# Optimization experiments

Hardware: AMD Instinct MI355X
Metric: run time of the kernel (lower is better)

Reference implementation:

```python
import jax, jax.numpy as jnp
import numpy as np
from jax import lax

B, T, S, D = 16, 16, 196, 768
H = 256          # hidden_dim
NH = 4           # attention heads
TH = 32          # temporal hidden = max(16, H//8)
UP = 4           # UPSAMPLE_FACTOR


def _ln(x, w, b):
    m = jnp.mean(x, -1, keepdims=True)
    v = jnp.mean((x - m) ** 2, -1, keepdims=True)
    return (x - m) / jnp.sqrt(v + 1e-5) * w + b


def _gelu(x):
    return jax.nn.gelu(x, approximate=False)  # torch nn.GELU default (erf)


def _upmat(g, f):
    # torch F.interpolate bilinear, align_corners=False, as a [g*f, g] matrix
    g_up = g * f
    src = np.maximum((np.arange(g_up) + 0.5) / f - 0.5, 0.0)
    i0 = np.minimum(np.floor(src).astype(np.int64), g - 1)
    i1 = np.minimum(i0 + 1, g - 1)
    w1 = (src - i0).astype(np.float32)
    w0 = 1.0 - w1
    W = np.zeros((g_up, g), dtype=np.float32)
    np.add.at(W, (np.arange(g_up), i0), w0)
    np.add.at(W, (np.arange(g_up), i1), w1)
    return jnp.asarray(W)


def setup_inputs() -> dict:
    key = jax.random.key(0)
    ks = jax.random.split(key, 12)
    r = lambda i, shape: jax.random.normal(ks[i], shape, jnp.float32) * 0.02
    return dict(
        tokens=jax.random.normal(ks[0], (B, T * S, D), jnp.float32),
        num_frames=T,
        fixed_box_wh=jax.random.uniform(ks[1], (2,), jnp.float32, 0.1, 0.5),
        ln_w=jnp.ones((D,), jnp.float32), ln_b=jnp.zeros((D,), jnp.float32),
        query=r(2, (1, 1, D)),
        in_proj_w=r(3, (3 * D, D)), in_proj_b=jnp.zeros((3 * D,), jnp.float32),
        out_w=r(4, (D, D)), out_b=jnp.zeros((D,), jnp.float32),
        an_w=jnp.ones((D,), jnp.float32), an_b=jnp.zeros((D,), jnp.float32),
        obj_w=r(5, (1, D)), obj_b=jnp.zeros((1,), jnp.float32),
        temperature=jnp.asarray(8.0, jnp.float32),
        r1_w=r(6, (H, 2 * D)), r1_b=jnp.zeros((H,), jnp.float32),
        r2_w=r(7, (H // 2, H)), r2_b=jnp.zeros((H // 2,), jnp.float32),
        r3_w=r(8, (2, H // 2)), r3_b=jnp.zeros((2,), jnp.float32),
        tc1_w=r(9, (TH, 2, 5)), tc1_b=jnp.zeros((TH,), jnp.float32),
        tc2_w=r(10, (2, TH, 5)), tc2_b=jnp.zeros((2,), jnp.float32),
    )


def reference(tokens, num_frames, fixed_box_wh, ln_w, ln_b, query,
              in_proj_w, in_proj_b, out_w, out_b, an_w, an_b, obj_w, obj_b,
              temperature, r1_w, r1_b, r2_w, r2_b, r3_w, r3_b,
              tc1_w, tc1_b, tc2_w, tc2_b):
    Bb, N, Dd = tokens.shape
    Tt = int(num_frames)
    Ss = N // Tt
    g = int(round(Ss ** 0.5))
    g_up = g * UP
    BT = Bb * Tt
    dt = tokens.dtype

    normed = _ln(tokens, ln_w, ln_b)
    flat = normed.reshape(BT, Ss, Dd)  # per-frame tokens

    # --- attention pooling with learned query (dropout off, eval) ---
    Wq, Wk, Wv = jnp.split(in_proj_w, 3, 0)
    bq, bk, bv = jnp.split(in_proj_b, 3, 0)
    dh = Dd // NH
    qh = (query.reshape(1, Dd) @ Wq.T + bq).reshape(NH, dh)  # same query for all frames
    kh = (flat @ Wk.T + bk).reshape(BT, Ss, NH, dh)
    vh = (flat @ Wv.T + bv).reshape(BT, Ss, NH, dh)
    scores = jnp.einsum('hd,bshd->bhs', qh, kh) / jnp.sqrt(jnp.asarray(dh, dt))
    attnp = jax.nn.softmax(scores, -1)
    ctx = jnp.einsum('bhs,bshd->bhd', attnp, vh).reshape(BT, Dd)
    pooled = _ln(ctx @ out_w.T + out_b, an_w, an_b)

    obj = (flat @ obj_w.T + obj_b)[..., 0]  # [BT,S]
    Wu = _upmat(g, UP)
    up = jnp.einsum('ug,bgh,vh->buv', Wu, obj.reshape(BT, g, g), Wu)
    up = up.reshape(BT, g_up * g_up)
    temp = jnp.maximum(temperature, 1.0)
    probs = jax.nn.softmax(up * temp, -1)
    coords = (jnp.arange(g_up, dtype=dt) + 0.5) / g_up
    yy, xx = jnp.meshgrid(coords, coords, indexing='ij')
    cx0 = probs @ xx.reshape(-1)
    cy0 = probs @ yy.reshape(-1)

    # --- 3x3 local token gather around coarse center ---
    cxg = jnp.clip(cx0 * g, 0, g - 1).astype(jnp.int32)
    cyg = jnp.clip(cy0 * g, 0, g - 1).astype(jnp.int32)
    off = jnp.array([-1, 0, 1], jnp.int32)
    gy = jnp.clip(cyg[:, None, None] + off[None, :, None], 0, g - 1)
    gx = jnp.clip(cxg[:, None, None] + off[None, None, :], 0, g - 1)
    idx = (gy * g + gx).reshape(BT, 9)
    local = jnp.take_along_axis(flat, idx[:, :, None], axis=1).mean(1)

    # --- refine MLP ---
    h1 = _gelu(jnp.concatenate([pooled, local], -1) @ r1_w.T + r1_b)
    h2 = _gelu(h1 @ r2_w.T + r2_b)
    delta = h2 @ r3_w.T + r3_b
    cx = jnp.clip(cx0 + 0.3 * jnp.tanh(delta[:, 0]), 0.0, 1.0)
    cy = jnp.clip(cy0 + 0.3 * jnp.tanh(delta[:, 1]), 0.0, 1.0)

    # --- temporal residual refiner over center trajectories ---
    seq = jnp.stack([cx, cy], 1).reshape(Bb, Tt, 2).transpose(0, 2, 1)  # [B,2,T]
    dn = ('NCH', 'OIH', 'NCH')
    t1 = _gelu(lax.conv_general_dilated(seq, tc1_w, (1,), [(2, 2)],
                                        dimension_numbers=dn) + tc1_b[None, :, None])
    td = lax.conv_general_dilated(t1, tc2_w, (1,), [(2, 2)],
                                  dimension_numbers=dn) + tc2_b[None, :, None]
    td = td.transpose(0, 2, 1).reshape(BT, 2)
    cx = jnp.clip(cx + 0.12 * jnp.tanh(td[:, 0]), 0.0, 1.0)
    cy = jnp.clip(cy + 0.12 * jnp.tanh(td[:, 1]), 0.0, 1.0)

    # --- fixed-size boxes ---
    min_size = 1.0 / g
    wh = jnp.clip(jnp.broadcast_to(fixed_box_wh.reshape(1, 2), (Bb, 2)), min_size, 1.0)
    wh = jnp.broadcast_to(wh[:, None, :], (Bb, Tt, 2)).reshape(BT, 2)
    w, h = wh[:, 0], wh[:, 1]
    x1 = jnp.clip(cx - 0.5 * w, 0.0, 1.0)
    y1 = jnp.clip(cy - 0.5 * h, 0.0, 1.0)
    x2 = jnp.clip(cx + 0.5 * w, 0.0, 1.0)
    y2 = jnp.clip(cy + 0.5 * h, 0.0, 1.0)
    x2 = jnp.clip(jnp.maximum(x2, x1 + min_size), 0.0, 1.0)
    y2 = jnp.clip(jnp.maximum(y2, y1 + min_size), 0.0, 1.0)
    return jnp.stack([x1, y1, x2, y2], 1).reshape(Bb, Tt, 4)
```

## Files before the change

### kernel.cpp

```cpp
#include <hip/hip_runtime.h>
#include <hip/hip_bf16.h>
#include <math.h>

#define SS 196
#define DD 768

__device__ __forceinline__ float b2f(ushort u){
  union { unsigned int i; float f; } v; v.i = ((unsigned int)u) << 16; return v.f;
}
__device__ __forceinline__ bool bfmode(const void* lnw){
  return ((const ushort*)lnw)[0] != 0;
}
__device__ __forceinline__ float ldx(const void* p, size_t i, bool bf){
  return bf ? b2f(((const ushort*)p)[i]) : ((const float*)p)[i];
}
__device__ __forceinline__ float gelu_f(float x){
  return 0.5f * x * (1.0f + erff(x * 0.70710678118654752f));
}
__device__ __forceinline__ float wredsum(float v){
  #pragma unroll
  for(int o=32;o;o>>=1) v += __shfl_xor(v,o,64);
  return v;
}
__device__ __forceinline__ float wredmax(float v){
  #pragma unroll
  for(int o=32;o;o>>=1) v = fmaxf(v, __shfl_xor(v,o,64));
  return v;
}

__global__ __launch_bounds__(256) void k_wkpart(const void* __restrict__ wproj,
                                                const void* __restrict__ query,
                                                const void* __restrict__ bproj,
                                                const void* __restrict__ flagp,
                                                float* __restrict__ wkp){
  bool bf = bfmode(flagp);
  int bx = blockIdx.x, c = blockIdx.y;
  int tid = threadIdx.x;
  int wv = tid>>6, lane = tid&63;
  int h = bx/3;
  __shared__ float sqh[12];
  #pragma unroll
  for(int j = wv*3; j < wv*3+3; j++){
    int rr = h*192 + c*12 + j;
    float acc = 0.f;
    #pragma unroll
    for(int i=0;i<12;i++){ int d = lane + 64*i; acc += ldx(query,d,bf) * ldx(wproj,(size_t)rr*DD+d,bf); }
    acc = wredsum(acc);
    if(lane==0) sqh[j] = acc + ldx(bproj, rr, bf);
  }
  __syncthreads();
  int idx = bx*256 + tid;
  int d = idx - h*DD;
  size_t base = ((size_t)(DD + h*192 + c*12))*DD + d;
  float acc = 0.f;
  #pragma unroll
  for(int j=0;j<12;j++) acc += sqh[j] * ldx(wproj, base + (size_t)j*DD, bf);
  wkp[(size_t)c*3072 + idx] = acc;
}

__global__ __launch_bounds__(256) void k_wkcomb(const float* __restrict__ wkp,
                                                const void* __restrict__ lnw,
                                                const void* __restrict__ lnb,
                                                const void* __restrict__ objw,
                                                float* __restrict__ wkraw,
                                                float* __restrict__ wf,
                                                float* __restrict__ s12p){
  bool bf = bfmode(lnw);
  int bx = blockIdx.x;
  int idx = bx*256 + threadIdx.x;
  int h = idx / DD, d = idx - h*DD;
  float s = 0.f;
  #pragma unroll
  for(int c=0;c<16;c++) s += wkp[(size_t)c*3072 + idx];
  wkraw[idx] = s;
  float w = ldx(lnw,d,bf);
  float wfv = w * s;
  wf[idx] = wfv;
  float lb = ldx(lnb,d,bf);
  float p0 = wfv;
  float p5 = lb * s;
  float p4 = 0.f, p9 = 0.f;
  if(bx < 3){
    float ow = ldx(objw,d,bf);
    float wfo = w * ow;
    wf[4*DD + d] = wfo;
    p4 = wfo;
    p9 = lb * ow;
  }
  p0 = wredsum(p0); p5 = wredsum(p5); p4 = wredsum(p4); p9 = wredsum(p9);
  __shared__ float red[4][4];
  int wv = threadIdx.x>>6, lane = threadIdx.x&63;
  if(lane==0){ red[0][wv]=p0; red[1][wv]=p5; red[2][wv]=p4; red[3][wv]=p9; }
  __syncthreads();
  if(threadIdx.x==0){
    float q0=red[0][0]+red[0][1]+red[0][2]+red[0][3];
    float q5=red[1][0]+red[1][1]+red[1][2]+red[1][3];
    float q4=red[2][0]+red[2][1]+red[2][2]+red[2][3];
    float q9=red[3][0]+red[3][1]+red[3][2]+red[3][3];
    #pragma unroll
    for(int r=0;r<10;r++) s12p[bx*10+r]=0.f;
    s12p[bx*10 + h] = q0;
    s12p[bx*10 + 5 + h] = q5;
    if(bx<3){ s12p[bx*10 + 4] = q4; s12p[bx*10 + 9] = q9; }
  }
}

__global__ __launch_bounds__(256) void k_pass1(const void* __restrict__ tok,
                                               const float* __restrict__ wf,
                                               const float* __restrict__ s12p,
                                               const void* __restrict__ objb,
                                               const void* __restrict__ flagp,
                                               float* __restrict__ scores,
                                               float* __restrict__ objv,
                                               float* __restrict__ meanv,
                                               float* __restrict__ rstdv){
  __shared__ __align__(16) float swf[5*DD];
  __shared__ float ss12[10];
  for(int i=threadIdx.x;i<5*DD;i+=256) swf[i]=wf[i];
  if(threadIdx.x<10){
    float a=0.f;
    #pragma unroll
    for(int b=0;b<12;b++) a += s12p[b*10+threadIdx.x];
    ss12[threadIdx.x]=a;
  }
  __syncthreads();
  bool bf = bfmode(flagp);
  int tid = threadIdx.x;
  int tl = tid & 15;
  int tkn = blockIdx.x*16 + (tid>>4);
  int f = tkn / SS, s = tkn - f*SS;
  float a0=0,a1=0,a2=0,a3=0,a4=0,sm=0,sq=0;
  if(bf){
    const ushort* x = (const ushort*)tok + (size_t)tkn * DD;
    #pragma unroll
    for(int i=0;i<12;i++){
      int d = 4*tl + 64*i;
      ushort4 u = *(const ushort4*)(x + d);
      float x0=b2f(u.x), x1=b2f(u.y), x2=b2f(u.z), x3=b2f(u.w);
      sm += (x0+x1)+(x2+x3); sq += (x0*x0+x1*x1)+(x2*x2+x3*x3);
      float4 w;
      w = *(const float4*)&swf[0*DD+d]; a0 += x0*w.x + x1*w.y + x2*w.z + x3*w.w;
      w = *(const float4*)&swf[1*DD+d]; a1 += x0*w.x + x1*w.y + x2*w.z + x3*w.w;
      w = *(const float4*)&swf[2*DD+d]; a2 += x0*w.x + x1*w.y + x2*w.z + x3*w.w;
      w = *(const float4*)&swf[3*DD+d]; a3 += x0*w.x + x1*w.y + x2*w.z + x3*w.w;
      w = *(const float4*)&swf[4*DD+d]; a4 += x0*w.x + x1*w.y + x2*w.z + x3*w.w;
    }
  } else {
    const float* x = (const float*)tok + (size_t)tkn * DD;
    #pragma unroll
    for(int i=0;i<12;i++){
      int d = 4*tl + 64*i;
      float4 u = *(const float4*)(x + d);
      sm += (u.x+u.y)+(u.z+u.w);
      sq += (u.x*u.x+u.y*u.y)+(u.z*u.z+u.w*u.w);
      float4 w;
      w = *(const float4*)&swf[0*DD+d]; a0 += u.x*w.x+u.y*w.y+u.z*w.z+u.w*w.w;
      w = *(const float4*)&swf[1*DD+d]; a1 += u.x*w.x+u.y*w.y+u.z*w.z+u.w*w.w;
      w = *(const float4*)&swf[2*DD+d]; a2 += u.x*w.x+u.y*w.y+u.z*w.z+u.w*w.w;
      w = *(const float4*)&swf[3*DD+d]; a3 += u.x*w.x+u.y*w.y+u.z*w.z+u.w*w.w;
      w = *(const float4*)&swf[4*DD+d]; a4 += u.x*w.x+u.y*w.y+u.z*w.z+u.w*w.w;
    }
  }
  #pragma unroll
  for(int o=8;o;o>>=1){
    sm += __shfl_xor(sm,o,64); sq += __shfl_xor(sq,o,64);
    a0 += __shfl_xor(a0,o,64); a1 += __shfl_xor(a1,o,64);
    a2 += __shfl_xor(a2,o,64); a3 += __shfl_xor(a3,o,64);
    a4 += __shfl_xor(a4,o,64);
  }
  if(tl==0){
    const float invD = 1.0f/768.0f;
    float m = sm*invD;
    float var = sq*invD - m*m;
    float rstd = rsqrtf(var + 1e-5f);
    meanv[tkn]=m; rstdv[tkn]=rstd;
    const float sc = 0.07216878364870322f;
    scores[(f*4+0)*SS+s] = (rstd*(a0 - m*ss12[0]) + ss12[5]) * sc;
    scores[(f*4+1)*SS+s] = (rstd*(a1 - m*ss12[1]) + ss12[6]) * sc;
    scores[(f*4+2)*SS+s] = (rstd*(a2 - m*ss12[2]) + ss12[7]) * sc;
    scores[(f*4+3)*SS+s] = (rstd*(a3 - m*ss12[3]) + ss12[8]) * sc;
    objv[tkn] = rstd*(a4 - m*ss12[4]) + ss12[9] + ldx(objb,0,bf);
  }
}

__global__ __launch_bounds__(512) void k_softobj(const void* __restrict__ tok,
                                                 float* __restrict__ aw,
                                                 const float* __restrict__ objv,
                                                 const float* __restrict__ meanv,
                                                 const float* __restrict__ rstdv,
                                                 const void* __restrict__ temp,
                                                 const void* __restrict__ lnw,
                                                 const void* __restrict__ lnb,
                                                 float* __restrict__ pl,
                                                 float* __restrict__ cterm,
                                                 float* __restrict__ cxy){
  bool bf = bfmode(lnw);
  int f = blockIdx.x, tid = threadIdx.x;
  int wv = tid >> 6, lane = tid & 63;
  __shared__ float sobj[196];
  __shared__ float up[3136];
  __shared__ int   i0a[56], i1a[56];
  __shared__ float w0a[56], w1a[56];
  __shared__ float redm[4], reds[8], redx[8], redy[8];
  __shared__ int   sidx[9];
  __shared__ float rj[9], rmj[9];
  if(tid<196) sobj[tid] = objv[(size_t)f*SS + tid];
  if(tid<56){
    float src = fmaxf((tid+0.5f)*0.25f - 0.5f, 0.0f);
    int i0 = min((int)floorf(src), 13);
    i0a[tid]=i0; i1a[tid]=min(i0+1,13);
    float w1 = src - (float)i0;
    w1a[tid]=w1; w0a[tid]=1.0f-w1;
  }
  __syncthreads();
  if(wv < 4){
    int h = wv;
    float* sc = aw + (size_t)(f*4+h)*SS;
    const float* rs = rstdv + f*SS;
    const float* mv = meanv + f*SS;
    float v[4]; float mx = -1e30f;
    #pragma unroll
    for(int j=0;j<4;j++){ int s=lane+64*j; v[j] = (s<SS)? sc[s] : -1e30f; mx=fmaxf(mx,v[j]); }
    mx = wredmax(mx);
    float e[4], sum=0.f;
    #pragma unroll
    for(int j=0;j<4;j++){ int s=lane+64*j; e[j] = (s<SS)? expf(v[j]-mx) : 0.f; sum += e[j]; }
    sum = wredsum(sum);
    float inv = 1.0f/sum;
    float cp = 0.f;
    #pragma unroll
    for(int j=0;j<4;j++){
      int s=lane+64*j;
      if(s<SS){ float r=rs[s]; float a=e[j]*inv*r; sc[s]=a; cp += a*mv[s]; }
    }
    cp = wredsum(cp);
    if(lane==0) cterm[f*4+h] = cp;
  } else {
    int w4 = wv-4;
    float lmax = -1e30f;
    for(int i = w4*64 + lane; i<3136; i+=256){
      int u=i/56, v=i-u*56;
      float val = w0a[u]*(w0a[v]*sobj[i0a[u]*14+i0a[v]] + w1a[v]*sobj[i0a[u]*14+i1a[v]])
                + w1a[u]*(w0a[v]*sobj[i1a[u]*14+i0a[v]] + w1a[v]*sobj[i1a[u]*14+i1a[v]]);
      up[i]=val; lmax=fmaxf(lmax,val);
    }
    lmax = wredmax(lmax);
    if(lane==0) redm[w4]=lmax;
  }
  __syncthreads();
  float mx = fmaxf(fmaxf(redm[0],redm[1]), fmaxf(redm[2],redm[3]));
  float t = fmaxf(ldx(temp,0,bf), 1.0f);
  float se=0, sx=0, sy=0;
  for(int i=tid;i<3136;i+=512){
    int u=i/56, v=i-u*56;
    float e = expf((up[i]-mx)*t);
    se += e;
    sx += e * ((v+0.5f)*(1.0f/56.0f));
    sy += e * ((u+0.5f)*(1.0f/56.0f));
  }
  se=wredsum(se); sx=wredsum(sx); sy=wredsum(sy);
  if(lane==0){ reds[wv]=se; redx[wv]=sx; redy[wv]=sy; }
  __syncthreads();
  se=0; sx=0; sy=0;
  #pragma unroll
  for(int i=0;i<8;i++){ se+=reds[i]; sx+=redx[i]; sy+=redy[i]; }
  float cx0 = sx/se, cy0 = sy/se;
  if(tid==0){ cxy[f*2]=cx0; cxy[f*2+1]=cy0; }
  float vx = fminf(fmaxf(cx0*14.0f,0.0f),13.0f); int cxg=(int)vx;
  float vy = fminf(fmaxf(cy0*14.0f,0.0f),13.0f); int cyg=(int)vy;
  if(tid<9){
    int dy = tid/3 - 1, dx = tid%3 - 1;
    int gy = min(max(cyg+dy,0),13), gx = min(max(cxg+dx,0),13);
    int s = gy*14+gx;
    sidx[tid]=s;
    float r = rstdv[(size_t)f*SS+s];
    rj[tid]=r; rmj[tid]=r*meanv[(size_t)f*SS+s];
  }
  __syncthreads();
  float offc = 0.f;
  #pragma unroll
  for(int j=0;j<9;j++) offc += rmj[j];
  for(int d=tid; d<DD; d+=512){
    float acc = 0.f;
    #pragma unroll
    for(int j=0;j<9;j++) acc += rj[j]*ldx(tok, (size_t)f*SS*DD + (size_t)sidx[j]*DD + d, bf);
    pl[(size_t)f*1536 + DD + d] = ldx(lnw,d,bf)*((acc-offc)*(1.0f/9.0f)) + ldx(lnb,d,bf);
  }
}

__global__ __launch_bounds__(256) void k_xbar_part(const void* __restrict__ tok,
                                                   const float* __restrict__ aw,
                                                   const void* __restrict__ flagp,
                                                   float* __restrict__ xpart){
  bool bf = bfmode(flagp);
  int f = blockIdx.x, c = blockIdx.y;
  __shared__ float a4[49*4];
  for(int i=threadIdx.x;i<49*4;i+=256){
    int s=i>>2, h=i&3;
    a4[i]=aw[(size_t)(f*4+h)*SS + c*49 + s];
  }
  __syncthreads();
  int tid = threadIdx.x;
  if(tid < 192){
    int d = tid*4;
    float4 A0={0,0,0,0},A1={0,0,0,0},A2={0,0,0,0},A3={0,0,0,0};
    if(bf){
      const ushort* tf = (const ushort*)tok + (size_t)(f*SS + c*49)*DD + d;
      #pragma unroll 7
      for(int s=0;s<49;s++){
        ushort4 u = *(const ushort4*)(tf + (size_t)s*DD);
        float x0=b2f(u.x), x1=b2f(u.y), x2=b2f(u.z), x3=b2f(u.w);
        float w0=a4[s*4+0], w1=a4[s*4+1], w2=a4[s*4+2], w3=a4[s*4+3];
        A0.x+=w0*x0; A0.y+=w0*x1; A0.z+=w0*x2; A0.w+=w0*x3;
        A1.x+=w1*x0; A1.y+=w1*x1; A1.z+=w1*x2; A1.w+=w1*x3;
        A2.x+=w2*x0; A2.y+=w2*x1; A2.z+=w2*x2; A2.w+=w2*x3;
        A3.x+=w3*x0; A3.y+=w3*x1; A3.z+=w3*x2; A3.w+=w3*x3;
      }
    } else {
      const float* tf = (const float*)tok + (size_t)(f*SS + c*49)*DD + d;
      #pragma unroll 7
      for(int s=0;s<49;s++){
        float4 u = *(const float4*)(tf + (size_t)s*DD);
        float w0=a4[s*4+0], w1=a4[s*4+1], w2=a4[s*4+2], w3=a4[s*4+3];
        A0.x+=w0*u.x; A0.y+=w0*u.y; A0.z+=w0*u.z; A0.w+=w0*u.w;
        A1.x+=w1*u.x; A1.y+=w1*u.y; A1.z+=w1*u.z; A1.w+=w1*u.w;
        A2.x+=w2*u.x; A2.y+=w2*u.y; A2.z+=w2*u.z; A2.w+=w2*u.w;
        A3.x+=w3*u.x; A3.y+=w3*u.y; A3.z+=w3*u.z; A3.w+=w3*u.w;
      }
    }
    size_t base = (((size_t)c*256 + f)*4)*DD + d;
    *(float4*)&xpart[base + 0*DD] = A0;
    *(float4*)&xpart[base + 1*DD] = A1;
    *(float4*)&xpart[base + 2*DD] = A2;
    *(float4*)&xpart[base + 3*DD] = A3;
  }
}

__global__ __launch_bounds__(256) void k_xbar_comb(const float* __restrict__ xpart,
                                                   const float* __restrict__ cterm,
                                                   const void* __restrict__ lnw,
                                                   const void* __restrict__ lnb,
                                                   float* __restrict__ xbar){
  bool bf = bfmode(lnw);
  int f = blockIdx.x;
  float c0=cterm[f*4+0], c1=cterm[f*4+1], c2=cterm[f*4+2], c3=cterm[f*4+3];
  #pragma unroll
  for(int j=0;j<3;j++){
    int d = threadIdx.x + 256*j;
    float w=ldx(lnw,d,bf), b=ldx(lnb,d,bf);
    float s0=0,s1=0,s2=0,s3=0;
    #pragma unroll
    for(int c=0;c<4;c++){
      size_t base = (((size_t)c*256 + f)*4)*DD + d;
      s0 += xpart[base + 0*DD];
      s1 += xpart[base + 1*DD];
      s2 += xpart[base + 2*DD];
      s3 += xpart[base + 3*DD];
    }
    xbar[((size_t)(f*4+0))*DD+d] = w*(s0-c0)+b;
    xbar[((size_t)(f*4+1))*DD+d] = w*(s1-c1)+b;
    xbar[((size_t)(f*4+2))*DD+d] = w*(s2-c2)+b;
    xbar[((size_t)(f*4+3))*DD+d] = w*(s3-c3)+b;
  }
}

template<int N, int K, int ACT, int CTX, int ROWOFF>
__global__ __launch_bounds__(256) void k_tgemm(const float* __restrict__ A,
                                               const void* __restrict__ W,
                                               const void* __restrict__ bias,
                                               const void* __restrict__ flagp,
                                               float* __restrict__ C){
  bool bf = bfmode(flagp);
  __shared__ float As[32][32];
  __shared__ float Bs[32][64];
  int tid = threadIdx.x;
  int n0 = blockIdx.x*64, m0 = blockIdx.y*32;
  int h  = n0 / 192;
  int am = tid>>3, ak = (tid&7)*4;
  int bn = tid>>2, bk = (tid&3)*8;
  const float* ap = A + (CTX ? ((size_t)((m0+am)*4+h))*768 : (size_t)(m0+am)*K) + ak;
  const ushort* wpb = (const ushort*)W + (size_t)(ROWOFF+n0+bn)*K + bk;
  const float*  wpf = (const float*)W  + (size_t)(ROWOFF+n0+bn)*K + bk;
  int tx = tid&15, ty = tid>>4;
  float acc[2][4] = {};
  float4 av; float b8[8];
  av = *(const float4*)ap;
  if(bf){
    ushort4 w0 = *(const ushort4*)(wpb);
    ushort4 w1 = *(const ushort4*)(wpb+4);
    b8[0]=b2f(w0.x); b8[1]=b2f(w0.y); b8[2]=b2f(w0.z); b8[3]=b2f(w0.w);
    b8[4]=b2f(w1.x); b8[5]=b2f(w1.y); b8[6]=b2f(w1.z); b8[7]=b2f(w1.w);
  } else {
    float4 w0 = *(const float4*)(wpf);
    float4 w1 = *(const float4*)(wpf+4);
    b8[0]=w0.x; b8[1]=w0.y; b8[2]=w0.z; b8[3]=w0.w;
    b8[4]=w1.x; b8[5]=w1.y; b8[6]=w1.z; b8[7]=w1.w;
  }
  for(int k0=0; k0<K; k0+=32){
    As[ak+0][am]=av.x; As[ak+1][am]=av.y; As[ak+2][am]=av.z; As[ak+3][am]=av.w;
    #pragma unroll
    for(int j=0;j<8;j++) Bs[bk+j][bn]=b8[j];
    __syncthreads();
    float4 av2; float b82[8];
    if(k0+32 < K){
      av2 = *(const float4*)(ap + k0 + 32);
      if(bf){
        ushort4 w0 = *(const ushort4*)(wpb + k0 + 32);
        ushort4 w1 = *(const ushort4*)(wpb + k0 + 36);
        b82[0]=b2f(w0.x); b82[1]=b2f(w0.y); b82[2]=b2f(w0.z); b82[3]=b2f(w0.w);
        b82[4]=b2f(w1.x); b82[5]=b2f(w1.y); b82[6]=b2f(w1.z); b82[7]=b2f(w1.w);
      } else {
        float4 w0 = *(const float4*)(wpf + k0 + 32);
        float4 w1 = *(const float4*)(wpf + k0 + 36);
        b82[0]=w0.x; b82[1]=w0.y; b82[2]=w0.z; b82[3]=w0.w;
        b82[4]=w1.x; b82[5]=w1.y; b82[6]=w1.z; b82[7]=w1.w;
      }
    }
    #pragma unroll
    for(int k=0;k<32;k++){
      float2 a = *(const float2*)&As[k][ty*2];
      float4 b = *(const float4*)&Bs[k][tx*4];
      acc[0][0]+=a.x*b.x; acc[0][1]+=a.x*b.y; acc[0][2]+=a.x*b.z; acc[0][3]+=a.x*b.w;
      acc[1][0]+=a.y*b.x; acc[1][1]+=a.y*b.y; acc[1][2]+=a.y*b.z; acc[1][3]+=a.y*b.w;
    }
    __syncthreads();
    av = av2;
    #pragma unroll
    for(int j=0;j<8;j++) b8[j]=b82[j];
  }
  int n = n0 + tx*4;
  float bv0=ldx(bias,ROWOFF+n,bf),   bv1=ldx(bias,ROWOFF+n+1,bf),
        bv2=ldx(bias,ROWOFF+n+2,bf), bv3=ldx(bias,ROWOFF+n+3,bf);
  #pragma unroll
  for(int i=0;i<2;i++){
    int m = m0 + ty*2 + i;
    float4 o;
    o.x=acc[i][0]+bv0; o.y=acc[i][1]+bv1; o.z=acc[i][2]+bv2; o.w=acc[i][3]+bv3;
    if(ACT){ o.x=gelu_f(o.x); o.y=gelu_f(o.y); o.z=gelu_f(o.z); o.w=gelu_f(o.w); }
    *(float4*)&C[(size_t)m*N + n] = o;
  }
}

__global__ __launch_bounds__(256) void k_lnan(const float* __restrict__ X,
                                              const void* __restrict__ anw,
                                              const void* __restrict__ anb,
                                              const void* __restrict__ flagp,
                                              float* __restrict__ pl){
  bool bf = bfmode(flagp);
  int wv = threadIdx.x >> 6, lane = threadIdx.x & 63;
  int f = blockIdx.x*4 + wv;
  const float* x = X + (size_t)f*DD;
  float v[12]; float sm=0, sq=0;
  #pragma unroll
  for(int i=0;i<12;i++){ v[i]=x[lane+64*i]; sm+=v[i]; sq+=v[i]*v[i]; }
  sm=wredsum(sm); sq=wredsum(sq);
  float m = sm*(1.0f/768.0f);
  float rstd = rsqrtf(sq*(1.0f/768.0f) - m*m + 1e-5f);
  #pragma unroll
  for(int i=0;i<12;i++){
    int d = lane+64*i;
    pl[(size_t)f*1536 + d] = (v[i]-m)*rstd*ldx(anw,d,bf) + ldx(anb,d,bf);
  }
}

__global__ __launch_bounds__(256) void k_final(const float* __restrict__ h2,
                                               const void* __restrict__ r3w,
                                               const void* __restrict__ r3b,
                                               const float* __restrict__ cxy,
                                               const void* __restrict__ tc1w,
                                               const void* __restrict__ tc1b,
                                               const void* __restrict__ tc2w,
                                               const void* __restrict__ tc2b,
                                               const void* __restrict__ fbw,
                                               const void* __restrict__ flagp,
                                               void* __restrict__ out){
  bool bf = bfmode(flagp);
  __shared__ float sxs[256], sys[256];
  __shared__ float t1[16*32*16];
  __shared__ float td[16*2*16];
  int f = threadIdx.x;
  float a0=0.f, a1=0.f;
  const float* hh = h2 + (size_t)f*128;
  for(int k=0;k<128;k++){ float x=hh[k]; a0 += x*ldx(r3w,k,bf); a1 += x*ldx(r3w,128+k,bf); }
  a0 += ldx(r3b,0,bf); a1 += ldx(r3b,1,bf);
  float cx1 = fminf(fmaxf(cxy[f*2]   + 0.3f*tanhf(a0), 0.f), 1.f);
  float cy1 = fminf(fmaxf(cxy[f*2+1] + 0.3f*tanhf(a1), 0.f), 1.f);
  sxs[f]=cx1; sys[f]=cy1;
  __syncthreads();
  for(int idx=f; idx<8192; idx+=256){
    int b = idx>>9, o = (idx>>4)&31, t = idx&15;
    float acc = ldx(tc1b,o,bf);
    #pragma unroll
    for(int k=0;k<5;k++){
      int tt = t + k - 2;
      if(tt>=0 && tt<16)
        acc += sxs[b*16+tt]*ldx(tc1w,o*10 + k,bf) + sys[b*16+tt]*ldx(tc1w,o*10 + 5 + k,bf);
    }
    t1[idx] = gelu_f(acc);
  }
  __syncthreads();
  for(int idx=f; idx<512; idx+=256){
    int b = idx>>5, c = (idx>>4)&1, t = idx&15;
    float acc = ldx(tc2b,c,bf);
    for(int o=0;o<32;o++){
      #pragma unroll
      for(int k=0;k<5;k++){
        int tt = t + k - 2;
        if(tt>=0 && tt<16) acc += t1[(b*32+o)*16+tt]*ldx(tc2w,(c*32+o)*5+k,bf);
      }
    }
    td[(b*2+c)*16+t] = acc;
  }
  __syncthreads();
  {
    int b = f>>4;
    float tdx = td[(b*2+0)*16+(f&15)], tdy = td[(b*2+1)*16+(f&15)];
    float cx2 = fminf(fmaxf(sxs[f] + 0.12f*tanhf(tdx), 0.f), 1.f);
    float cy2 = fminf(fmaxf(sys[f] + 0.12f*tanhf(tdy), 0.f), 1.f);
    const float ms = 1.0f/14.0f;
    float w  = fminf(fmaxf(ldx(fbw,0,bf), ms), 1.f);
    float ht = fminf(fmaxf(ldx(fbw,1,bf), ms), 1.f);
    float x1 = fminf(fmaxf(cx2 - 0.5f*w , 0.f), 1.f);
    float y1 = fminf(fmaxf(cy2 - 0.5f*ht, 0.f), 1.f);
    float x2 = fminf(fmaxf(cx2 + 0.5f*w , 0.f), 1.f);
    float y2 = fminf(fmaxf(cy2 + 0.5f*ht, 0.f), 1.f);
    x2 = fminf(fmaxf(fmaxf(x2, x1+ms), 0.f), 1.f);
    y2 = fminf(fmaxf(fmaxf(y2, y1+ms), 0.f), 1.f);
    if(bf){
      __hip_bfloat16* ob = (__hip_bfloat16*)out;
      ob[f*4+0]=__float2bfloat16(x1);
      ob[f*4+1]=__float2bfloat16(y1);
      ob[f*4+2]=__float2bfloat16(x2);
      ob[f*4+3]=__float2bfloat16(y2);
    } else {
      float* of = (float*)out;
      of[f*4+0]=x1; of[f*4+1]=y1; of[f*4+2]=x2; of[f*4+3]=y2;
    }
  }
}

extern "C" void kernel_launch(void* const* d_in, const int* in_sizes, int n_in,
                              void* d_out, int out_size, void* d_ws, size_t ws_size,
                              hipStream_t stream){
  (void)in_sizes; (void)n_in; (void)out_size; (void)ws_size;
  const void* tok   = d_in[0];
  const void* fbw   = d_in[2];
  const void* lnw   = d_in[3];
  const void* lnb   = d_in[4];
  const void* query = d_in[5];
  const void* wproj = d_in[6];
  const void* bproj = d_in[7];
  const void* outw  = d_in[8];
  const void* outb  = d_in[9];
  const void* anw   = d_in[10];
  const void* anb   = d_in[11];
  const void* objw  = d_in[12];
  const void* objb  = d_in[13];
  const void* temp  = d_in[14];
  const void* r1w   = d_in[15];
  const void* r1b   = d_in[16];
  const void* r2w   = d_in[17];
  const void* r2b   = d_in[18];
  const void* r3w   = d_in[19];
  const void* r3b   = d_in[20];
  const void* tc1w  = d_in[21];
  const void* tc1b  = d_in[22];
  const void* tc2w  = d_in[23];
  const void* tc2b  = d_in[24];

  float* ws    = (float*)d_ws;
  float* wkraw = ws;
  float* wf    = wkraw + 3072;
  float* s12p  = wf + 3840;
  float* wkp   = s12p + 128;
  float* scores= wkp + 49152;
  float* objv  = scores + 200704;
  float* meanv = objv + 50176;
  float* rstdv = meanv + 50176;
  float* cterm = rstdv + 50176;
  float* xbar  = cterm + 1024;
  float* ctx   = xbar + 786432;
  float* ppre  = ctx + 196608;
  float* pl    = ppre + 196608;
  float* h1    = pl + 393216;
  float* h2    = h1 + 65536;
  float* cxy   = h2 + 32768;
  float* xpart = cxy + 512;

  hipLaunchKernelGGL(k_wkpart, dim3(12,16),  dim3(256), 0, stream, wproj, query, bproj, lnw, wkp);
  hipLaunchKernelGGL(k_wkcomb, dim3(12),     dim3(256), 0, stream, wkp, lnw, lnb, objw, wkraw, wf, s12p);
  hipLaunchKernelGGL(k_pass1,  dim3(3136),   dim3(256), 0, stream, tok, wf, s12p, objb, lnw, scores, objv, meanv, rstdv);
  hipLaunchKernelGGL(k_softobj,dim3(256),    dim3(512), 0, stream, tok, scores, objv, meanv, rstdv, temp, lnw, lnb, pl, cterm, cxy);
  hipLaunchKernelGGL(k_xbar_part, dim3(256,4), dim3(256), 0, stream, tok, scores, lnw, xpart);
  hipLaunchKernelGGL(k_xbar_comb, dim3(256),   dim3(256), 0, stream, xpart, cterm, lnw, lnb, xbar);
  hipLaunchKernelGGL((k_tgemm<768,768,0,1,1536>), dim3(12,8), dim3(256), 0, stream, xbar, wproj, bproj, lnw, ctx);
  hipLaunchKernelGGL((k_tgemm<768,768,0,0,0>),    dim3(12,8), dim3(256), 0, stream, ctx, outw, outb, lnw, ppre);
  hipLaunchKernelGGL(k_lnan,   dim3(64),     dim3(256), 0, stream, ppre, anw, anb, lnw, pl);
  hipLaunchKernelGGL((k_tgemm<256,1536,1,0,0>), dim3(4,8), dim3(256), 0, stream, pl, r1w, r1b, lnw, h1);
  hipLaunchKernelGGL((k_tgemm<128,256,1,0,0>),  dim3(2,8), dim3(256), 0, stream, h1, r2w, r2b, lnw, h2);
  hipLaunchKernelGGL(k_final,  dim3(1),      dim3(256), 0, stream, h2, r3w, r3b, cxy, tc1w, tc1b, tc2w, tc2b, fbw, lnw, (void*)d_out);
}
```

Before: 505.1 us.

## Fuse softmax/objectness into xbar partial kernel and fold xbar combine into ctx GEMM

Merges the softmax/objectness kernel and the xbar partial-sum kernel into one launch with a (256,5) grid. Every block recomputes the per-head softmax weights into shared memory. Block c==0 handles the objectness upsample, centroid and local pooling, while the other blocks do the weighted token reductions. The xbar combine kernel is removed: the ctx GEMM now sums the four partials and applies the LN affine and cterm correction while loading its A tile. This drops two launches and the xbar round trip, at the cost of redundant softmax work and a heavier A-load in the GEMM.

Result: slower. 521.3 us (+3.2%).

```diff
diff --git a/kernel.cpp b/kernel.cpp
--- a/kernel.cpp
+++ b/kernel.cpp
@@ -183,39 +183,42 @@
   }
 }
 
-__global__ __launch_bounds__(512) void k_softobj(const void* __restrict__ tok,
-                                                 float* __restrict__ aw,
-                                                 const float* __restrict__ objv,
-                                                 const float* __restrict__ meanv,
-                                                 const float* __restrict__ rstdv,
-                                                 const void* __restrict__ temp,
-                                                 const void* __restrict__ lnw,
-                                                 const void* __restrict__ lnb,
-                                                 float* __restrict__ pl,
-                                                 float* __restrict__ cterm,
-                                                 float* __restrict__ cxy){
+__global__ __launch_bounds__(256) void k_attn(const void* __restrict__ tok,
+                                              const float* __restrict__ scores,
+                                              const float* __restrict__ objv,
+                                              const float* __restrict__ meanv,
+                                              const float* __restrict__ rstdv,
+                                              const void* __restrict__ temp,
+                                              const void* __restrict__ lnw,
+                                              const void* __restrict__ lnb,
+                                              float* __restrict__ xpart,
+                                              float* __restrict__ pl,
+                                              float* __restrict__ cterm,
+                                              float* __restrict__ cxy){
   bool bf = bfmode(lnw);
-  int f = blockIdx.x, tid = threadIdx.x;
-  int wv = tid >> 6, lane = tid & 63;
+  int f = blockIdx.x, c = blockIdx.y;
+  int tid = threadIdx.x, wv = tid>>6, lane = tid&63;
+  __shared__ float a4[SS*4];
   __shared__ float sobj[196];
   __shared__ float up[3136];
   __shared__ int   i0a[56], i1a[56];
   __shared__ float w0a[56], w1a[56];
-  __shared__ float redm[4], reds[8], redx[8], redy[8];
+  __shared__ float redm[4], reds[4], redx[4], redy[4];
   __shared__ int   sidx[9];
   __shared__ float rj[9], rmj[9];
-  if(tid<196) sobj[tid] = objv[(size_t)f*SS + tid];
-  if(tid<56){
-    float src = fmaxf((tid+0.5f)*0.25f - 0.5f, 0.0f);
-    int i0 = min((int)floorf(src), 13);
-    i0a[tid]=i0; i1a[tid]=min(i0+1,13);
-    float w1 = src - (float)i0;
-    w1a[tid]=w1; w0a[tid]=1.0f-w1;
-  }
-  __syncthreads();
-  if(wv < 4){
+  if(c==0){
+    if(tid<196) sobj[tid] = objv[(size_t)f*SS + tid];
+    if(tid<56){
+      float src = fmaxf((tid+0.5f)*0.25f - 0.5f, 0.0f);
+      int i0 = min((int)floorf(src), 13);
+      i0a[tid]=i0; i1a[tid]=min(i0+1,13);
+      float w1 = src - (float)i0;
+      w1a[tid]=w1; w0a[tid]=1.0f-w1;
+    }
+  }
+  {
     int h = wv;
-    float* sc = aw + (size_t)(f*4+h)*SS;
+    const float* sc = scores + (size_t)(f*4+h)*SS;
     const float* rs = rstdv + f*SS;
     const float* mv = meanv + f*SS;
     float v[4]; float mx = -1e30f;
@@ -231,136 +234,194 @@
     #pragma unroll
     for(int j=0;j<4;j++){
       int s=lane+64*j;
-      if(s<SS){ float r=rs[s]; float a=e[j]*inv*r; sc[s]=a; cp += a*mv[s]; }
+      if(s<SS){ float r=rs[s]; float a=e[j]*inv*r; a4[s*4+h]=a; cp += a*mv[s]; }
     }
     cp = wredsum(cp);
-    if(lane==0) cterm[f*4+h] = cp;
-  } else {
-    int w4 = wv-4;
+    if(c==0 && lane==0) cterm[f*4+h] = cp;
+  }
+  __syncthreads();
+  if(c==0){
     float lmax = -1e30f;
-    for(int i = w4*64 + lane; i<3136; i+=256){
+    for(int i=tid;i<3136;i+=256){
       int u=i/56, v=i-u*56;
       float val = w0a[u]*(w0a[v]*sobj[i0a[u]*14+i0a[v]] + w1a[v]*sobj[i0a[u]*14+i1a[v]])
                 + w1a[u]*(w0a[v]*sobj[i1a[u]*14+i0a[v]] + w1a[v]*sobj[i1a[u]*14+i1a[v]]);
       up[i]=val; lmax=fmaxf(lmax,val);
     }
     lmax = wredmax(lmax);
-    if(lane==0) redm[w4]=lmax;
-  }
-  __syncthreads();
-  float mx = fmaxf(fmaxf(redm[0],redm[1]), fmaxf(redm[2],redm[3]));
-  float t = fmaxf(ldx(temp,0,bf), 1.0f);
-  float se=0, sx=0, sy=0;
-  for(int i=tid;i<3136;i+=512){
-    int u=i/56, v=i-u*56;
-    float e = expf((up[i]-mx)*t);
-    se += e;
-    sx += e * ((v+0.5f)*(1.0f/56.0f));
-    sy += e * ((u+0.5f)*(1.0f/56.0f));
-  }
-  se=wredsum(se); sx=wredsum(sx); sy=wredsum(sy);
-  if(lane==0){ reds[wv]=se; redx[wv]=sx; redy[wv]=sy; }
-  __syncthreads();
-  se=0; sx=0; sy=0;
-  #pragma unroll
-  for(int i=0;i<8;i++){ se+=reds[i]; sx+=redx[i]; sy+=redy[i]; }
-  float cx0 = sx/se, cy0 = sy/se;
-  if(tid==0){ cxy[f*2]=cx0; cxy[f*2+1]=cy0; }
-  float vx = fminf(fmaxf(cx0*14.0f,0.0f),13.0f); int cxg=(int)vx;
-  float vy = fminf(fmaxf(cy0*14.0f,0.0f),13.0f); int cyg=(int)vy;
-  if(tid<9){
-    int dy = tid/3 - 1, dx = tid%3 - 1;
-    int gy = min(max(cyg+dy,0),13), gx = min(max(cxg+dx,0),13);
-    int s = gy*14+gx;
-    sidx[tid]=s;
-    float r = rstdv[(size_t)f*SS+s];
-    rj[tid]=r; rmj[tid]=r*meanv[(size_t)f*SS+s];
-  }
-  __syncthreads();
-  float offc = 0.f;
-  #pragma unroll
-  for(int j=0;j<9;j++) offc += rmj[j];
-  for(int d=tid; d<DD; d+=512){
-    float acc = 0.f;
-    #pragma unroll
-    for(int j=0;j<9;j++) acc += rj[j]*ldx(tok, (size_t)f*SS*DD + (size_t)sidx[j]*DD + d, bf);
-    pl[(size_t)f*1536 + DD + d] = ldx(lnw,d,bf)*((acc-offc)*(1.0f/9.0f)) + ldx(lnb,d,bf);
-  }
-}
-
-__global__ __launch_bounds__(256) void k_xbar_part(const void* __restrict__ tok,
-                                                   const float* __restrict__ aw,
-                                                   const void* __restrict__ flagp,
-                                                   float* __restrict__ xpart){
-  bool bf = bfmode(flagp);
-  int f = blockIdx.x, c = blockIdx.y;
-  __shared__ float a4[49*4];
-  for(int i=threadIdx.x;i<49*4;i+=256){
-    int s=i>>2, h=i&3;
-    a4[i]=aw[(size_t)(f*4+h)*SS + c*49 + s];
-  }
-  __syncthreads();
-  int tid = threadIdx.x;
-  if(tid < 192){
-    int d = tid*4;
-    float4 A0={0,0,0,0},A1={0,0,0,0},A2={0,0,0,0},A3={0,0,0,0};
-    if(bf){
-      const ushort* tf = (const ushort*)tok + (size_t)(f*SS + c*49)*DD + d;
-      #pragma unroll 7
-      for(int s=0;s<49;s++){
-        ushort4 u = *(const ushort4*)(tf + (size_t)s*DD);
-        float x0=b2f(u.x), x1=b2f(u.y), x2=b2f(u.z), x3=b2f(u.w);
-        float w0=a4[s*4+0], w1=a4[s*4+1], w2=a4[s*4+2], w3=a4[s*4+3];
-        A0.x+=w0*x0; A0.y+=w0*x1; A0.z+=w0*x2; A0.w+=w0*x3;
-        A1.x+=w1*x0; A1.y+=w1*x1; A1.z+=w1*x2; A1.w+=w1*x3;
-        A2.x+=w2*x0; A2.y+=w2*x1; A2.z+=w2*x2; A2.w+=w2*x3;
-        A3.x+=w3*x0; A3.y+=w3*x1; A3.z+=w3*x2; A3.w+=w3*x3;
+    if(lane==0) redm[wv]=lmax;
+    __syncthreads();
+    float mx = fmaxf(fmaxf(redm[0],redm[1]), fmaxf(redm[2],redm[3]));
+    float t = fmaxf(ldx(temp,0,bf), 1.0f);
+    float se=0, sx=0, sy=0;
+    for(int i=tid;i<3136;i+=256){
+      int u=i/56, v=i-u*56;
+      float e = expf((up[i]-mx)*t);
+      se += e;
+      sx += e * ((v+0.5f)*(1.0f/56.0f));
+      sy += e * ((u+0.5f)*(1.0f/56.0f));
+    }
+    se=wredsum(se); sx=wredsum(sx); sy=wredsum(sy);
+    if(lane==0){ reds[wv]=se; redx[wv]=sx; redy[wv]=sy; }
+    __syncthreads();
+    se=reds[0]+reds[1]+reds[2]+reds[3];
+    sx=redx[0]+redx[1]+redx[2]+redx[3];
+    sy=redy[0]+redy[1]+redy[2]+redy[3];
+    float cx0 = sx/se, cy0 = sy/se;
+    if(tid==0){ cxy[f*2]=cx0; cxy[f*2+1]=cy0; }
+    float vx = fminf(fmaxf(cx0*14.0f,0.0f),13.0f); int cxg=(int)vx;
+    float vy = fminf(fmaxf(cy0*14.0f,0.0f),13.0f); int cyg=(int)vy;
+    if(tid<9){
+      int dy = tid/3 - 1, dx = tid%3 - 1;
+      int gy = min(max(cyg+dy,0),13), gx = min(max(cxg+dx,0),13);
+      int s = gy*14+gx;
+      sidx[tid]=s;
+      float r = rstdv[(size_t)f*SS+s];
+      rj[tid]=r; rmj[tid]=r*meanv[(size_t)f*SS+s];
+    }
+    __syncthreads();
+    float offc = 0.f;
+    #pragma unroll
+    for(int j=0;j<9;j++) offc += rmj[j];
+    for(int d=tid; d<DD; d+=256){
+      float acc = 0.f;
+      #pragma unroll
+      for(int j=0;j<9;j++) acc += rj[j]*ldx(tok, (size_t)f*SS*DD + (size_t)sidx[j]*DD + d, bf);
+      pl[(size_t)f*1536 + DD + d] = ldx(lnw,d,bf)*((acc-offc)*(1.0f/9.0f)) + ldx(lnb,d,bf);
+    }
+  } else {
+    int cc = c-1;
+    if(tid < 192){
+      int d = tid*4;
+      float4 A0={0,0,0,0},A1={0,0,0,0},A2={0,0,0,0},A3={0,0,0,0};
+      const float* wp = &a4[cc*49*4];
+      if(bf){
+        const ushort* tf = (const ushort*)tok + (size_t)(f*SS + cc*49)*DD + d;
+        #pragma unroll 7
+        for(int s=0;s<49;s++){
+          ushort4 u = *(const ushort4*)(tf + (size_t)s*DD);
+          float x0=b2f(u.x), x1=b2f(u.y), x2=b2f(u.z), x3=b2f(u.w);
+          float w0=wp[s*4+0], w1=wp[s*4+1], w2=wp[s*4+2], w3=wp[s*4+3];
+          A0.x+=w0*x0; A0.y+=w0*x1; A0.z+=w0*x2; A0.w+=w0*x3;
+          A1.x+=w1*x0; A1.y+=w1*x1; A1.z+=w1*x2; A1.w+=w1*x3;
+          A2.x+=w2*x0; A2.y+=w2*x1; A2.z+=w2*x2; A2.w+=w2*x3;
+          A3.x+=w3*x0; A3.y+=w3*x1; A3.z+=w3*x2; A3.w+=w3*x3;
+        }
+      } else {
+        const float* tf = (const float*)tok + (size_t)(f*SS + cc*49)*DD + d;
+        #pragma unroll 7
+        for(int s=0;s<49;s++){
+          float4 u = *(const float4*)(tf + (size_t)s*DD);
+          float w0=wp[s*4+0], w1=wp[s*4+1], w2=wp[s*4+2], w3=wp[s*4+3];
+          A0.x+=w0*u.x; A0.y+=w0*u.y; A0.z+=w0*u.z; A0.w+=w0*u.w;
+          A1.x+=w1*u.x; A1.y+=w1*u.y; A1.z+=w1*u.z; A1.w+=w1*u.w;
+          A2.x+=w2*u.x; A2.y+=w2*u.y; A2.z+=w2*u.z; A2.w+=w2*u.w;
+          A3.x+=w3*u.x; A3.y+=w3*u.y; A3.z+=w3*u.z; A3.w+=w3*u.w;
+        }
       }
-    } else {
-      const float* tf = (const float*)tok + (size_t)(f*SS + c*49)*DD + d;
-      #pragma unroll 7
-      for(int s=0;s<49;s++){
-        float4 u = *(const float4*)(tf + (size_t)s*DD);
-        float w0=a4[s*4+0], w1=a4[s*4+1], w2=a4[s*4+2], w3=a4[s*4+3];
-        A0.x+=w0*u.x; A0.y+=w0*u.y; A0.z+=w0*u.z; A0.w+=w0*u.w;
-        A1.x+=w1*u.x; A1.y+=w1*u.y; A1.z+=w1*u.z; A1.w+=w1*u.w;
-        A2.x+=w2*u.x; A2.y+=w2*u.y; A2.z+=w2*u.z; A2.w+=w2*u.w;
-        A3.x+=w3*u.x; A3.y+=w3*u.y; A3.z+=w3*u.z; A3.w+=w3*u.w;
-      }
-    }
-    size_t base = (((size_t)c*256 + f)*4)*DD + d;
-    *(float4*)&xpart[base + 0*DD] = A0;
-    *(float4*)&xpart[base + 1*DD] = A1;
-    *(float4*)&xpart[base + 2*DD] = A2;
-    *(float4*)&xpart[base + 3*DD] = A3;
-  }
-}
-
-__global__ __launch_bounds__(256) void k_xbar_comb(const float* __restrict__ xpart,
+      size_t base = (((size_t)cc*256 + f)*4)*DD + d;
+      *(float4*)&xpart[base + 0*DD] = A0;
+      *(float4*)&xpart[base + 1*DD] = A1;
+      *(float4*)&xpart[base + 2*DD] = A2;
+      *(float4*)&xpart[base + 3*DD] = A3;
+    }
+  }
+}
+
+__global__ __launch_bounds__(256) void k_tgemm_ctx(const float* __restrict__ xpart,
                                                    const float* __restrict__ cterm,
+                                                   const void* __restrict__ W,
+                                                   const void* __restrict__ bias,
                                                    const void* __restrict__ lnw,
                                                    const void* __restrict__ lnb,
-                                                   float* __restrict__ xbar){
-  bool bf = bfmode(lnw);
-  int f = blockIdx.x;
-  float c0=cterm[f*4+0], c1=cterm[f*4+1], c2=cterm[f*4+2], c3=cterm[f*4+3];
-  #pragma unroll
-  for(int j=0;j<3;j++){
-    int d = threadIdx.x + 256*j;
-    float w=ldx(lnw,d,bf), b=ldx(lnb,d,bf);
-    float s0=0,s1=0,s2=0,s3=0;
-    #pragma unroll
-    for(int c=0;c<4;c++){
-      size_t base = (((size_t)c*256 + f)*4)*DD + d;
-      s0 += xpart[base + 0*DD];
-      s1 += xpart[base + 1*DD];
-      s2 += xpart[base + 2*DD];
-      s3 += xpart[base + 3*DD];
-    }
-    xbar[((size_t)(f*4+0))*DD+d] = w*(s0-c0)+b;
-    xbar[((size_t)(f*4+1))*DD+d] = w*(s1-c1)+b;
-    xbar[((size_t)(f*4+2))*DD+d] = w*(s2-c2)+b;
-    xbar[((size_t)(f*4+3))*DD+d] = w*(s3-c3)+b;
+                                                   const void* __restrict__ flagp,
+                                                   float* __restrict__ C){
+  const int K = 768, N = 768, ROWOFF = 1536;
+  bool bf = bfmode(flagp);
+  __shared__ float As[32][32];
+  __shared__ float Bs[32][64];
+  int tid = threadIdx.x;
+  int n0 = blockIdx.x*64, m0 = blockIdx.y*32;
+  int h  = n0 / 192;
+  int am = tid>>3, ak = (tid&7)*4;
+  int bn = tid>>2, bk = (tid&3)*8;
+  int frame = m0 + am;
+  float ct = cterm[frame*4 + h];
+  const float* x0p = xpart + ((size_t)frame*4 + h)*DD + ak;
+  const size_t CS = (size_t)256*4*DD;
+  const ushort* wpb = (const ushort*)W + (size_t)(ROWOFF+n0+bn)*K + bk;
+  const float*  wpf = (const float*)W  + (size_t)(ROWOFF+n0+bn)*K + bk;
+  int tx = tid&15, ty = tid>>4;
+  float acc[2][4] = {};
+  float4 av; float b8[8];
+  auto loadA = [&](int k0)->float4 {
+    float4 p0 = *(const float4*)(x0p + k0);
+    float4 p1 = *(const float4*)(x0p + CS + k0);
+    float4 p2 = *(const float4*)(x0p + 2*CS + k0);
+    float4 p3 = *(const float4*)(x0p + 3*CS + k0);
+    float4 s;
+    s.x=((p0.x+p1.x)+p2.x)+p3.x; s.y=((p0.y+p1.y)+p2.y)+p3.y;
+    s.z=((p0.z+p1.z)+p2.z)+p3.z; s.w=((p0.w+p1.w)+p2.w)+p3.w;
+    int d = ak + k0;
+    s.x = ldx(lnw,d+0,bf)*(s.x-ct)+ldx(lnb,d+0,bf);
+    s.y = ldx(lnw,d+1,bf)*(s.y-ct)+ldx(lnb,d+1,bf);
+    s.z = ldx(lnw,d+2,bf)*(s.z-ct)+ldx(lnb,d+2,bf);
+    s.w = ldx(lnw,d+3,bf)*(s.w-ct)+ldx(lnb,d+3,bf);
+    return s;
+  };
+  av = loadA(0);
+  if(bf){
+    ushort4 w0 = *(const ushort4*)(wpb);
+    ushort4 w1 = *(const ushort4*)(wpb+4);
+    b8[0]=b2f(w0.x); b8[1]=b2f(w0.y); b8[2]=b2f(w0.z); b8[3]=b2f(w0.w);
+    b8[4]=b2f(w1.x); b8[5]=b2f(w1.y); b8[6]=b2f(w1.z); b8[7]=b2f(w1.w);
+  } else {
+    float4 w0 = *(const float4*)(wpf);
+    float4 w1 = *(const float4*)(wpf+4);
+    b8[0]=w0.x; b8[1]=w0.y; b8[2]=w0.z; b8[3]=w0.w;
+    b8[4]=w1.x; b8[5]=w1.y; b8[6]=w1.z; b8[7]=w1.w;
+  }
+  for(int k0=0; k0<K; k0+=32){
+    As[ak+0][am]=av.x; As[ak+1][am]=av.y; As[ak+2][am]=av.z; As[ak+3][am]=av.w;
+    #pragma unroll
+    for(int j=0;j<8;j++) Bs[bk+j][bn]=b8[j];
+    __syncthreads();
+    float4 av2={0,0,0,0}; float b82[8];
+    if(k0+32 < K){
+      av2 = loadA(k0+32);
+      if(bf){
+        ushort4 w0 = *(const ushort4*)(wpb + k0 + 32);
+        ushort4 w1 = *(const ushort4*)(wpb + k0 + 36);
+        b82[0]=b2f(w0.x); b82[1]=b2f(w0.y); b82[2]=b2f(w0.z); b82[3]=b2f(w0.w);
+        b82[4]=b2f(w1.x); b82[5]=b2f(w1.y); b82[6]=b2f(w1.z); b82[7]=b2f(w1.w);
+      } else {
+        float4 w0 = *(const float4*)(wpf + k0 + 32);
+        float4 w1 = *(const float4*)(wpf + k0 + 36);
+        b82[0]=w0.x; b82[1]=w0.y; b82[2]=w0.z; b82[3]=w0.w;
+        b82[4]=w1.x; b82[5]=w1.y; b82[6]=w1.z; b82[7]=w1.w;
+      }
+    }
+    #pragma unroll
+    for(int k=0;k<32;k++){
+      float2 a = *(const float2*)&As[k][ty*2];
+      float4 b = *(const float4*)&Bs[k][tx*4];
+      acc[0][0]+=a.x*b.x; acc[0][1]+=a.x*b.y; acc[0][2]+=a.x*b.z; acc[0][3]+=a.x*b.w;
+      acc[1][0]+=a.y*b.x; acc[1][1]+=a.y*b.y; acc[1][2]+=a.y*b.z; acc[1][3]+=a.y*b.w;
+    }
+    __syncthreads();
+    av = av2;
+    #pragma unroll
+    for(int j=0;j<8;j++) b8[j]=b82[j];
+  }
+  int n = n0 + tx*4;
+  float bv0=ldx(bias,ROWOFF+n,bf),   bv1=ldx(bias,ROWOFF+n+1,bf),
+        bv2=ldx(bias,ROWOFF+n+2,bf), bv3=ldx(bias,ROWOFF+n+3,bf);
+  #pragma unroll
+  for(int i=0;i<2;i++){
+    int m = m0 + ty*2 + i;
+    float4 o;
+    o.x=acc[i][0]+bv0; o.y=acc[i][1]+bv1; o.z=acc[i][2]+bv2; o.w=acc[i][3]+bv3;
+    *(float4*)&C[(size_t)m*N + n] = o;
   }
 }
 
@@ -578,8 +639,7 @@
   float* meanv = objv + 50176;
   float* rstdv = meanv + 50176;
   float* cterm = rstdv + 50176;
-  float* xbar  = cterm + 1024;
-  float* ctx   = xbar + 786432;
+  float* ctx   = cterm + 1024;
   float* ppre  = ctx + 196608;
   float* pl    = ppre + 196608;
   float* h1    = pl + 393216;
@@ -590,11 +650,9 @@
   hipLaunchKernelGGL(k_wkpart, dim3(12,16),  dim3(256), 0, stream, wproj, query, bproj, lnw, wkp);
   hipLaunchKernelGGL(k_wkcomb, dim3(12),     dim3(256), 0, stream, wkp, lnw, lnb, objw, wkraw, wf, s12p);
   hipLaunchKernelGGL(k_pass1,  dim3(3136),   dim3(256), 0, stream, tok, wf, s12p, objb, lnw, scores, objv, meanv, rstdv);
-  hipLaunchKernelGGL(k_softobj,dim3(256),    dim3(512), 0, stream, tok, scores, objv, meanv, rstdv, temp, lnw, lnb, pl, cterm, cxy);
-  hipLaunchKernelGGL(k_xbar_part, dim3(256,4), dim3(256), 0, stream, tok, scores, lnw, xpart);
-  hipLaunchKernelGGL(k_xbar_comb, dim3(256),   dim3(256), 0, stream, xpart, cterm, lnw, lnb, xbar);
-  hipLaunchKernelGGL((k_tgemm<768,768,0,1,1536>), dim3(12,8), dim3(256), 0, stream, xbar, wproj, bproj, lnw, ctx);
-  hipLaunchKernelGGL((k_tgemm<768,768,0,0,0>),    dim3(12,8), dim3(256), 0, stream, ctx, outw, outb, lnw, ppre);
+  hipLaunchKernelGGL(k_attn,   dim3(256,5),  dim3(256), 0, stream, tok, scores, objv, meanv, rstdv, temp, lnw, lnb, xpart, pl, cterm, cxy);
+  hipLaunchKernelGGL(k_tgemm_ctx, dim3(12,8), dim3(256), 0, stream, xpart, cterm, wproj, bproj, lnw, lnb, lnw, ctx);
+  hipLaunchKernelGGL((k_tgemm<768,768,0,0,0>), dim3(12,8), dim3(256), 0, stream, ctx, outw, outb, lnw, ppre);
   hipLaunchKernelGGL(k_lnan,   dim3(64),     dim3(256), 0, stream, ppre, anw, anb, lnw, pl);
   hipLaunchKernelGGL((k_tgemm<256,1536,1,0,0>), dim3(4,8), dim3(256), 0, stream, pl, r1w, r1b, lnw, h1);
   hipLaunchKernelGGL((k_tgemm<128,256,1,0,0>),  dim3(2,8), dim3(256), 0, stream, h1, r2w, r2b, lnw, h2);
```
